# Kernel tuning notes

Measured on AMD Instinct MI355X. Metric: run time of the kernel, lower is better.

The kernel has to match this reference:

```python
import jax, jax.numpy as jnp
import numpy as np

WS = (5, 3, 1)          # per-level window sizes (CrossLayerPosEmbedding3D default)
STRIDES = (4, 2, 1)
PADS = (2, 1, 0)
HWS = (80, 40, 20)      # per-level map sizes -> 20x20 = 400 windows per level
B, C, NH = 8, 256, 4
HD = C // NH            # head_dim = 64
NTOK = (25, 9, 1)       # tokens per level, total 35
W0 = WS[0]
TABLE = (2 * W0 - 1) ** 2  # 81


def _rel_pos_index():
    # replicates CrossLayerPosEmbedding3D (spatial=True): float cross-scale coords
    coords = []
    for i, w in enumerate(WS):
        c = (np.arange(w) - w // 2).astype(np.float64)
        if i < len(WS) - 1:
            c = c * (W0 / w)
        gh, gw = np.meshgrid(c, c, indexing='ij')
        coords.append(np.stack([gh.reshape(-1), gw.reshape(-1)]))
    cf = np.concatenate(coords, axis=-1)                       # (2, 35)
    rel = (cf[:, :, None] - cf[:, None, :]).transpose(1, 2, 0).copy()
    rel[..., 0] += W0 - 1
    rel[..., 1] += W0 - 1
    rel[..., 0] *= 2 * W0 - 1
    return rel.sum(-1).astype(np.float32)                      # (35, 35) float index

REL_IDX = _rel_pos_index()
LEVEL_OF_TOKEN = np.repeat(np.arange(3), NTOK)                 # (35,)


def unfold(x, k, s, p):
    # torch.nn.functional.unfold -> (B, n_windows, k*k, C) (overlaped_window_partition)
    Bx, Cx, H, W = x.shape
    xp = jnp.pad(x, ((0, 0), (0, 0), (p, p), (p, p)))
    oh = (H + 2 * p - k) // s + 1
    ow = (W + 2 * p - k) // s + 1
    hi = (np.arange(oh) * s)[:, None] + np.arange(k)           # (oh, k)
    wi = (np.arange(ow) * s)[:, None] + np.arange(k)           # (ow, k)
    pt = xp[:, :, hi[:, None, :, None], wi[None, :, None, :]]  # (B, C, oh, ow, k, k)
    return pt.transpose(0, 2, 3, 4, 5, 1).reshape(Bx, oh * ow, k * k, Cx)


def fold(win, H, W, k, s, p):
    # torch.nn.functional.fold (sums overlaps) (overlaped_window_reverse)
    Bx, Wm, _, Cx = win.shape
    oh = (H + 2 * p - k) // s + 1
    ow = (W + 2 * p - k) // s + 1
    Hp, Wp = H + 2 * p, W + 2 * p
    hi = (np.arange(oh) * s)[:, None] + np.arange(k)
    wi = (np.arange(ow) * s)[:, None] + np.arange(k)
    lin = (hi[:, None, :, None] * Wp + wi[None, :, None, :]).reshape(-1)
    vals = win.transpose(0, 3, 1, 2).reshape(Bx, Cx, -1)       # matches (Wm, k*k) flatten order
    canvas = jnp.zeros((Bx, Cx, Hp * Wp), win.dtype).at[:, :, lin].add(vals)
    return canvas.reshape(Bx, Cx, Hp, Wp)[:, :, p:p + H, p:p + W]


def _l2n(x):
    # F.normalize(dim=-1), eps=1e-12
    return x / jnp.maximum(jnp.linalg.norm(x, axis=-1, keepdims=True), 1e-12)


def _forward(x0, x1, x2, w_qkv0, w_qkv1, w_qkv2, w_proj, b_proj, rpb_table, abs_bias):
    xs = (x0, x1, x2)
    wq = (w_qkv0, w_qkv1, w_qkv2)
    qs, ks, vs = [], [], []
    for l in range(3):  # small fixed layer loop (structurally distinct weights)
        t = unfold(xs[l], WS[l], STRIDES[l], PADS[l])          # (B, 400, ws^2, C)
        qkv = jnp.einsum('bwtc,cf->bwtf', t, wq[l])
        Bx, Wm, T, _ = qkv.shape
        qkv = qkv.reshape(Bx, Wm, T, 3, NH, HD).transpose(3, 0, 4, 1, 2, 5)  # (3,B,H,Wm,t,hd)
        qs.append(qkv[0]); ks.append(qkv[1]); vs.append(qkv[2])
    q = jnp.concatenate(qs, axis=-2)                           # (B, H, 400, 35, hd)
    k = jnp.concatenate(ks, axis=-2)
    v = jnp.concatenate(vs, axis=-2)

    # interpolated cross-layer relative position bias (floor/ceil lerp on the table)
    idx = jnp.asarray(REL_IDX.reshape(-1))
    fl = jnp.clip(jnp.floor(idx).astype(jnp.int32), 0, TABLE - 1)
    ce = jnp.clip(jnp.ceil(idx).astype(jnp.int32), 0, TABLE - 1)
    wce = (idx - fl.astype(jnp.float32))[:, None]
    pos = (1.0 - wce) * rpb_table[fl] + wce * rpb_table[ce]    # (1225, NH)
    pos = pos.reshape(sum(NTOK), sum(NTOK), NH).transpose(2, 0, 1)  # (NH, 35, 35)
    # per-level absolute bias added on query-row blocks (torch cat over dim=-2)
    pos = pos + abs_bias[LEVEL_OF_TOKEN].T[:, :, None]

    attn = jnp.einsum('bhwqd,bhwkd->bhwqk', _l2n(q), _l2n(k)) + pos[None, :, None]
    attn = jax.nn.softmax(attn, axis=-1)
    out = jnp.einsum('bhwqk,bhwkd->bhwqd', attn, v)            # (B, H, 400, 35, hd)
    Bx = out.shape[0]
    out = out.transpose(0, 2, 3, 1, 4).reshape(Bx, -1, sum(NTOK), NH * HD)  # (B,400,35,C)
    out = jnp.einsum('bwtc,cf->bwtf', out, w_proj) + b_proj
    outs = jnp.split(out, np.cumsum(NTOK)[:-1].tolist(), axis=2)
    return tuple(fold(o, HWS[l], HWS[l], WS[l], STRIDES[l], PADS[l])
                 for l, o in enumerate(outs))


def setup_inputs() -> dict:
    key = jax.random.key(0)
    ks = jax.random.split(key, 8)
    return {
        'x0': jax.random.normal(ks[0], (B, C, 80, 80), jnp.float32),
        'x1': jax.random.normal(ks[1], (B, C, 40, 40), jnp.float32),
        'x2': jax.random.normal(ks[2], (B, C, 20, 20), jnp.float32),
        'w_qkv0': jax.random.normal(ks[3], (C, 3 * C), jnp.float32) * 0.02,
        'w_qkv1': jax.random.normal(ks[4], (C, 3 * C), jnp.float32) * 0.02,
        'w_qkv2': jax.random.normal(ks[5], (C, 3 * C), jnp.float32) * 0.02,
        'w_proj': jax.random.normal(ks[6], (C, C), jnp.float32) * 0.02,
        'b_proj': jnp.zeros((C,), jnp.float32),
        'rpb_table': jax.random.normal(ks[7], (TABLE, NH), jnp.float32) * 0.02,
        'abs_bias': jnp.zeros((3, NH), jnp.float32),
    }


def reference(x0, x1, x2, w_qkv0, w_qkv1, w_qkv2, w_proj, b_proj, rpb_table, abs_bias):
    return _forward(x0, x1, x2, w_qkv0, w_qkv1, w_qkv2, w_proj, b_proj, rpb_table, abs_bias)
```

## Files before the change

kernel.cpp:

```cpp
#include <hip/hip_runtime.h>
#include <math.h>

namespace {

typedef _Float16 half8v __attribute__((ext_vector_type(8)));
typedef _Float16 half4v __attribute__((ext_vector_type(4)));
typedef float    floatx4 __attribute__((ext_vector_type(4)));

constexpr int B   = 8;
constexpr int C   = 256;
constexpr int NH  = 4;
constexpr int HD  = 64;
constexpr int NWIN = 400;
constexpr int NT  = 35;
constexpr int QKVN = 768;
constexpr int RPB = NWIN * NT;

constexpr size_t QKV_B  = (size_t)8400 * QKVN * 2;
constexpr size_t OATT_B = (size_t)RPB * C * 2;
constexpr size_t YT_B   = (size_t)RPB * C * 4;
constexpr size_t PB_B   = QKV_B + OATT_B + YT_B;
constexpr size_t POS_B  = 19712;

__device__ inline unsigned pack2(float a, float b) {
  union { _Float16 h[2]; unsigned u; } x;
  x.h[0] = (_Float16)a; x.h[1] = (_Float16)b;
  return x.u;
}

__device__ inline void token_coord(int j, double& cy, double& cx) {
  if (j < 25)      { int ty = j / 5,  tx = j % 5;  cy = (double)(ty - 2); cx = (double)(tx - 2); }
  else if (j < 34) { int t = j - 25; int ty = t / 3, tx = t % 3;
                     cy = (double)(ty - 1) * (5.0 / 3.0); cx = (double)(tx - 1) * (5.0 / 3.0); }
  else             { cy = 0.0; cx = 0.0; }
}

__global__ void pos_kernel(const float* __restrict__ rpb, const float* __restrict__ ab,
                           float* __restrict__ pos) {
  int p = blockIdx.x * blockDim.x + threadIdx.x;
  if (p >= NH * NT * NT) return;
  int j = p % NT, i = (p / NT) % NT, h = p / (NT * NT);
  double cyi, cxi, cyj, cxj;
  token_coord(i, cyi, cxi);
  token_coord(j, cyj, cxj);
  float fidx = (float)(((cyi - cyj) + 4.0) * 9.0 + ((cxi - cxj) + 4.0));
  int fl = min(max((int)floorf(fidx), 0), 80);
  int ce = min(max((int)ceilf(fidx), 0), 80);
  float w = fidx - (float)fl;
  float pv = (1.0f - w) * rpb[fl * NH + h] + w * rpb[ce * NH + h];
  int li = (i < 25) ? 0 : ((i < 34) ? 1 : 2);
  pos[p] = pv + ab[li * NH + h];
}

__global__ __launch_bounds__(256) void qkv_gemm(const float* __restrict__ X,
                                                const float* __restrict__ W,
                                                _Float16* __restrict__ Y,
                                                int HW, int Mg, int normN) {
  __shared__ _Float16 As[128][40];
  __shared__ _Float16 Bs[128][40];
  const int tid  = threadIdx.x;
  const int m0   = blockIdx.x * 128;
  const int n0   = blockIdx.y * 128;
  const int w    = tid >> 6;
  const int lane = tid & 63;
  const int quad = lane >> 4;
  const int mn   = lane & 15;

  floatx4 acc[2][8] = {};
  for (int k0 = 0; k0 < C; k0 += 32) {
    float av[2][8], bv[2][8];
    int rl[2];
#pragma unroll
    for (int u = 0; u < 2; ++u) {
      int c = w * 2 + u;
      int ko = c & 3;
      rl[u] = (c >> 2) * 64 + lane;
      int gm = min(m0 + rl[u], Mg - 1);
      int bb = gm / HW, pix = gm - bb * HW;
      const float* xp = X + ((size_t)bb * C + k0 + ko * 8) * HW + pix;
#pragma unroll
      for (int j = 0; j < 8; ++j) av[u][j] = xp[(size_t)j * HW];
      const float* wp = W + (size_t)(k0 + ko * 8) * QKVN + n0 + rl[u];
#pragma unroll
      for (int j = 0; j < 8; ++j) bv[u][j] = wp[(size_t)j * QKVN];
    }
#pragma unroll
    for (int u = 0; u < 2; ++u) {
      int ko = (w * 2 + u) & 3;
      half8v ha, hb;
#pragma unroll
      for (int j = 0; j < 8; ++j) { ha[j] = (_Float16)av[u][j]; hb[j] = (_Float16)bv[u][j]; }
      *(half8v*)&As[rl[u]][ko * 8] = ha;
      *(half8v*)&Bs[rl[u]][ko * 8] = hb;
    }
    __syncthreads();
    half8v a0 = *(const half8v*)&As[w * 32 + mn][quad * 8];
    half8v a1 = *(const half8v*)&As[w * 32 + 16 + mn][quad * 8];
#pragma unroll
    for (int ni = 0; ni < 8; ++ni) {
      half8v bf = *(const half8v*)&Bs[ni * 16 + mn][quad * 8];
      acc[0][ni] = __builtin_amdgcn_mfma_f32_16x16x32_f16(a0, bf, acc[0][ni], 0, 0, 0);
      acc[1][ni] = __builtin_amdgcn_mfma_f32_16x16x32_f16(a1, bf, acc[1][ni], 0, 0, 0);
    }
    __syncthreads();
  }

  const bool do_norm = (n0 < normN);
#pragma unroll
  for (int mi = 0; mi < 2; ++mi) {
#pragma unroll
    for (int r = 0; r < 4; ++r) {
      float s0 = 0.f, s1 = 0.f;
#pragma unroll
      for (int ni = 0; ni < 4; ++ni) { float vv = acc[mi][ni][r]; s0 += vv * vv; }
#pragma unroll
      for (int ni = 4; ni < 8; ++ni) { float vv = acc[mi][ni][r]; s1 += vv * vv; }
      s0 += __shfl_xor(s0, 1); s1 += __shfl_xor(s1, 1);
      s0 += __shfl_xor(s0, 2); s1 += __shfl_xor(s1, 2);
      s0 += __shfl_xor(s0, 4); s1 += __shfl_xor(s1, 4);
      s0 += __shfl_xor(s0, 8); s1 += __shfl_xor(s1, 8);
      float sc0 = do_norm ? (1.f / fmaxf(sqrtf(s0), 1e-12f)) : 1.f;
      float sc1 = do_norm ? (1.f / fmaxf(sqrtf(s1), 1e-12f)) : 1.f;
      int row = m0 + w * 32 + mi * 16 + quad * 4 + r;
      if (row < Mg) {
#pragma unroll
        for (int ni = 0; ni < 8; ++ni)
          Y[(size_t)row * QKVN + n0 + ni * 16 + mn] =
              (_Float16)(acc[mi][ni][r] * (ni < 4 ? sc0 : sc1));
      }
    }
  }
}

__device__ inline const _Float16* token_row_ptr(int j, int wy, int wx, int b,
                                                const _Float16* q0, const _Float16* q1,
                                                const _Float16* q2) {
  if (j >= NT) return nullptr;
  int k_, s_, p_, Hl, t; const _Float16* base;
  if (j < 25)      { k_ = 5; s_ = 4; p_ = 2; Hl = 80; t = j;      base = q0; }
  else if (j < 34) { k_ = 3; s_ = 2; p_ = 1; Hl = 40; t = j - 25; base = q1; }
  else             { k_ = 1; s_ = 1; p_ = 0; Hl = 20; t = 0;      base = q2; }
  int ty = t / k_, tx = t % k_;
  int y = wy * s_ + ty - p_;
  int x = wx * s_ + tx - p_;
  if ((unsigned)y >= (unsigned)Hl || (unsigned)x >= (unsigned)Hl) return nullptr;
  return base + ((size_t)b * Hl * Hl + (size_t)y * Hl + x) * QKVN;
}

__global__ __launch_bounds__(256, 4) void attn_kernel(const _Float16* __restrict__ qkv0,
                                                      const _Float16* __restrict__ qkv1,
                                                      const _Float16* __restrict__ qkv2,
                                                      const float* __restrict__ pos,
                                                      _Float16* __restrict__ O) {
  const int blk = blockIdx.x;
  const int w   = blk % NWIN;
  const int b   = blk / NWIN;
  const int wy = w / 20, wx = w % 20;
  const int tid  = threadIdx.x;
  const int h    = tid >> 6;
  const int lane = tid & 63;
  const int i16  = lane & 15;
  const int q4   = lane >> 4;

  __shared__ __align__(16) _Float16 vrows[48][260];

#pragma unroll
  for (int e0 = 0; e0 < 1536; e0 += 256) {
    int e = e0 + tid;
    int j = e >> 5, cc = e & 31;
    half8v val = (half8v)(_Float16)0.f;
    if (j < NT) {
      const _Float16* rp = token_row_ptr(j, wy, wx, b, qkv0, qkv1, qkv2);
      if (rp) val = *(const half8v*)(rp + 512 + cc * 8);
    }
    *(half8v*)&vrows[j][cc * 8] = val;
  }

  half8v qf[3][2], kf[3][2];
#pragma unroll
  for (int t = 0; t < 3; ++t) {
    const _Float16* rp = token_row_ptr(t * 16 + i16, wy, wx, b, qkv0, qkv1, qkv2);
#pragma unroll
    for (int kc = 0; kc < 2; ++kc) {
      if (rp) {
        qf[t][kc] = *(const half8v*)(rp + h * HD + kc * 32 + q4 * 8);
        kf[t][kc] = *(const half8v*)(rp + 256 + h * HD + kc * 32 + q4 * 8);
      } else {
        qf[t][kc] = (half8v)(_Float16)0.f;
        kf[t][kc] = (half8v)(_Float16)0.f;
      }
    }
  }

  floatx4 s[3][3] = {};
#pragma unroll
  for (int kc = 0; kc < 2; ++kc)
#pragma unroll
    for (int tj = 0; tj < 3; ++tj)
#pragma unroll
      for (int ti = 0; ti < 3; ++ti)
        s[tj][ti] = __builtin_amdgcn_mfma_f32_16x16x32_f16(kf[tj][kc], qf[ti][kc], s[tj][ti], 0, 0, 0);

#pragma unroll
  for (int tj = 0; tj < 3; ++tj)
#pragma unroll
    for (int ti = 0; ti < 3; ++ti)
#pragma unroll
      for (int r = 0; r < 4; ++r) {
        int j = tj * 16 + q4 * 4 + r;
        int i = ti * 16 + i16;
        if (j < NT) { if (i < NT) s[tj][ti][r] += pos[(h * NT + i) * NT + j]; }
        else s[tj][ti][r] = -INFINITY;
      }

  half4v pa[3][3];
#pragma unroll
  for (int ti = 0; ti < 3; ++ti) {
    float m = s[0][ti][0];
#pragma unroll
    for (int tj = 0; tj < 3; ++tj)
#pragma unroll
      for (int r = 0; r < 4; ++r) m = fmaxf(m, s[tj][ti][r]);
    m = fmaxf(m, __shfl_xor(m, 16));
    m = fmaxf(m, __shfl_xor(m, 32));
    float sum = 0.f;
#pragma unroll
    for (int tj = 0; tj < 3; ++tj)
#pragma unroll
      for (int r = 0; r < 4; ++r) { float e = expf(s[tj][ti][r] - m); s[tj][ti][r] = e; sum += e; }
    sum += __shfl_xor(sum, 16);
    sum += __shfl_xor(sum, 32);
    float inv = 1.f / sum;
#pragma unroll
    for (int tj = 0; tj < 3; ++tj)
#pragma unroll
      for (int r = 0; r < 4; ++r) pa[tj][ti][r] = (_Float16)(s[tj][ti][r] * inv);
  }

  __syncthreads();

  half4v vb[3][4];
#pragma unroll
  for (int tj = 0; tj < 3; ++tj)
#pragma unroll
    for (int n = 0; n < 4; ++n)
#pragma unroll
      for (int kk = 0; kk < 4; ++kk)
        vb[tj][n][kk] = vrows[tj * 16 + q4 * 4 + kk][h * HD + n * 16 + i16];

  const size_t obase = ((size_t)(b * NWIN + w) * NT) * C + h * HD;
#pragma unroll
  for (int ti = 0; ti < 3; ++ti) {
    floatx4 o[4] = {};
#pragma unroll
    for (int tj = 0; tj < 3; ++tj)
#pragma unroll
      for (int n = 0; n < 4; ++n)
        o[n] = __builtin_amdgcn_mfma_f32_16x16x16f16(pa[tj][ti], vb[tj][n], o[n], 0, 0, 0);
#pragma unroll
    for (int r = 0; r < 4; ++r) {
      int i = ti * 16 + q4 * 4 + r;
      if (i < NT) {
#pragma unroll
        for (int n = 0; n < 4; ++n)
          O[obase + (size_t)i * C + n * 16 + i16] = (_Float16)o[n][r];
      }
    }
  }
}

__global__ __launch_bounds__(256) void proj_gemm(const _Float16* __restrict__ A,
                                                 const float* __restrict__ W,
                                                 const float* __restrict__ bias,
                                                 float* __restrict__ Yt, int Mg) {
  __shared__ __align__(16) char smem[128 * 69 * 4];
  _Float16 (*As)[40] = (_Float16(*)[40])smem;
  _Float16 (*Bs)[40] = (_Float16(*)[40])(smem + 128 * 40 * 2);
  float    (*Cs)[69] = (float(*)[69])smem;

  const int tid  = threadIdx.x;
  const int m0   = blockIdx.x * 128;
  const int n0   = blockIdx.y * 64;
  const int w    = tid >> 6;
  const int lane = tid & 63;
  const int quad = lane >> 4;
  const int mn   = lane & 15;

  floatx4 acc[2][4] = {};
  for (int k0 = 0; k0 < C; k0 += 32) {
#pragma unroll
    for (int u = 0; u < 2; ++u) {
      int e = u * 256 + tid;
      int m = e >> 2, k8 = e & 3;
      int row = min(m0 + m, Mg - 1);
      half8v va = *(const half8v*)&A[(size_t)row * C + k0 + 8 * k8];
      *(half8v*)&As[m][8 * k8] = va;
    }
    {
      const float* wp = W + (size_t)(k0 + w * 8) * C + n0 + lane;
      float wv[8];
#pragma unroll
      for (int j = 0; j < 8; ++j) wv[j] = wp[(size_t)j * C];
      half8v hv;
#pragma unroll
      for (int j = 0; j < 8; ++j) hv[j] = (_Float16)wv[j];
      *(half8v*)&Bs[lane][w * 8] = hv;
    }
    __syncthreads();
    half8v a0 = *(const half8v*)&As[w * 32 + mn][quad * 8];
    half8v a1 = *(const half8v*)&As[w * 32 + 16 + mn][quad * 8];
#pragma unroll
    for (int ni = 0; ni < 4; ++ni) {
      half8v bf = *(const half8v*)&Bs[ni * 16 + mn][quad * 8];
      acc[0][ni] = __builtin_amdgcn_mfma_f32_16x16x32_f16(a0, bf, acc[0][ni], 0, 0, 0);
      acc[1][ni] = __builtin_amdgcn_mfma_f32_16x16x32_f16(a1, bf, acc[1][ni], 0, 0, 0);
    }
    __syncthreads();
  }

#pragma unroll
  for (int mi = 0; mi < 2; ++mi)
#pragma unroll
    for (int r = 0; r < 4; ++r)
#pragma unroll
      for (int ni = 0; ni < 4; ++ni)
        Cs[w * 32 + mi * 16 + quad * 4 + r][ni * 16 + mn] =
            acc[mi][ni][r] + bias[n0 + ni * 16 + mn];
  __syncthreads();
#pragma unroll
  for (int u = 0; u < 32; ++u) {
    int e = u * 256 + tid;
    int ml = e & 127, cl = e >> 7;
    int m = m0 + ml;
    if (m < Mg) {
      int bb = m / RPB;
      int r = m - bb * RPB;
      Yt[((size_t)bb * C + n0 + cl) * RPB + r] = Cs[ml][cl];
    }
  }
}

__global__ __launch_bounds__(256) void fold_kernel(const float* __restrict__ Yt,
                                                   float* __restrict__ out,
                                                   int k_, int s_, int p_, int H_,
                                                   int toff, int total) {
  int idx = blockIdx.x * 256 + threadIdx.x;
  if (idx >= total) return;
  int x = idx % H_;
  int y = (idx / H_) % H_;
  int c = (idx / (H_ * H_)) % C;
  int b = idx / (C * H_ * H_);
  int py = y + p_, px = x + p_;
  int ay = py - k_ + 1;
  int wy_lo = ay <= 0 ? 0 : (ay + s_ - 1) / s_;
  int wy_hi = min(19, py / s_);
  int ax = px - k_ + 1;
  int wx_lo = ax <= 0 ? 0 : (ax + s_ - 1) / s_;
  int wx_hi = min(19, px / s_);
  const float* base = Yt + ((size_t)b * C + c) * RPB;
  float acc = 0.f;
  for (int wy = wy_lo; wy <= wy_hi; ++wy) {
    int tyy = py - wy * s_;
    for (int wx = wx_lo; wx <= wx_hi; ++wx) {
      int txx = px - wx * s_;
      acc += base[(wy * 20 + wx) * NT + toff + tyy * k_ + txx];
    }
  }
  out[idx] = acc;
}

}

extern "C" void kernel_launch(void* const* d_in, const int* in_sizes, int n_in,
                              void* d_out, int out_size, void* d_ws, size_t ws_size,
                              hipStream_t stream) {
  const float* x0    = (const float*)d_in[0];
  const float* x1    = (const float*)d_in[1];
  const float* x2    = (const float*)d_in[2];
  const float* wq0   = (const float*)d_in[3];
  const float* wq1   = (const float*)d_in[4];
  const float* wq2   = (const float*)d_in[5];
  const float* wproj = (const float*)d_in[6];
  const float* bproj = (const float*)d_in[7];
  const float* rpb   = (const float*)d_in[8];
  const float* ab    = (const float*)d_in[9];
  float* out = (float*)d_out;

  int g = 8;
  while (g > 1 && POS_B + (size_t)g * PB_B > ws_size) g >>= 1;

  char* ws = (char*)d_ws;
  float*    posb  = (float*)ws;
  _Float16* qkv0g = (_Float16*)(ws + POS_B);
  _Float16* qkv1g = qkv0g + (size_t)g * 6400 * QKVN;
  _Float16* qkv2g = qkv1g + (size_t)g * 1600 * QKVN;
  _Float16* oatt  = qkv2g + (size_t)g *  400 * QKVN;
  float*    yt    = (float*)(ws + POS_B + (size_t)g * (QKV_B + OATT_B));

  pos_kernel<<<(NH * NT * NT + 255) / 256, 256, 0, stream>>>(rpb, ab, posb);

  const size_t off1 = (size_t)B * C * 6400;
  const size_t off2 = off1 + (size_t)B * C * 1600;

  for (int b0 = 0; b0 < B; b0 += g) {
    const float* x0g = x0 + (size_t)b0 * C * 6400;
    const float* x1g = x1 + (size_t)b0 * C * 1600;
    const float* x2g = x2 + (size_t)b0 * C * 400;

    qkv_gemm<<<dim3((g * 6400 + 127) / 128, QKVN / 128), 256, 0, stream>>>(x0g, wq0, qkv0g, 6400, g * 6400, 512);
    qkv_gemm<<<dim3((g * 1600 + 127) / 128, QKVN / 128), 256, 0, stream>>>(x1g, wq1, qkv1g, 1600, g * 1600, 512);
    qkv_gemm<<<dim3((g *  400 + 127) / 128, QKVN / 128), 256, 0, stream>>>(x2g, wq2, qkv2g,  400, g *  400, 512);

    attn_kernel<<<g * NWIN, 256, 0, stream>>>(qkv0g, qkv1g, qkv2g, posb, oatt);

    proj_gemm<<<dim3((g * RPB + 127) / 128, C / 64), 256, 0, stream>>>(oatt, wproj, bproj, yt, g * RPB);

    const int tot0 = g * C * 6400;
    const int tot1 = g * C * 1600;
    const int tot2 = g * C * 400;
    fold_kernel<<<(tot0 + 255) / 256, 256, 0, stream>>>(yt, out + (size_t)b0 * C * 6400,        5, 4, 2, 80, 0,  tot0);
    fold_kernel<<<(tot1 + 255) / 256, 256, 0, stream>>>(yt, out + off1 + (size_t)b0 * C * 1600, 3, 2, 1, 40, 25, tot1);
    fold_kernel<<<(tot2 + 255) / 256, 256, 0, stream>>>(yt, out + off2 + (size_t)b0 * C * 400,  1, 1, 0, 20, 34, tot2);
  }
}
```

Before: 493.5 us.

## Merge per-level QKV GEMMs into one launch and prefetch next K-tile in GEMMs

Combines the three per-level QKV GEMM launches into a single grid that picks its level's input, weights and output from the block index. This cuts launch overhead and lets the small level-1/2 tiles fill gaps alongside level 0. Both the QKV and projection GEMMs now load the next K-slice from global memory into registers while MFMAs run on the current LDS tile, so global latency is hidden behind compute. The cost is higher register pressure, which may reduce occupancy.

```diff
diff --git a/kernel.cpp b/kernel.cpp
--- a/kernel.cpp
+++ b/kernel.cpp
@@ -21,12 +21,6 @@
 constexpr size_t YT_B   = (size_t)RPB * C * 4;
 constexpr size_t PB_B   = QKV_B + OATT_B + YT_B;
 constexpr size_t POS_B  = 19712;
-
-__device__ inline unsigned pack2(float a, float b) {
-  union { _Float16 h[2]; unsigned u; } x;
-  x.h[0] = (_Float16)a; x.h[1] = (_Float16)b;
-  return x.u;
-}
 
 __device__ inline void token_coord(int j, double& cy, double& cx) {
   if (j < 25)      { int ty = j / 5,  tx = j % 5;  cy = (double)(ty - 2); cx = (double)(tx - 2); }
@@ -52,48 +46,72 @@
   pos[p] = pv + ab[li * NH + h];
 }
 
-__global__ __launch_bounds__(256) void qkv_gemm(const float* __restrict__ X,
-                                                const float* __restrict__ W,
-                                                _Float16* __restrict__ Y,
-                                                int HW, int Mg, int normN) {
+__global__ __launch_bounds__(256) void qkv_gemm(const float* __restrict__ X0,
+                                                const float* __restrict__ X1,
+                                                const float* __restrict__ X2,
+                                                const float* __restrict__ W0,
+                                                const float* __restrict__ W1,
+                                                const float* __restrict__ W2,
+                                                _Float16* __restrict__ Y0,
+                                                _Float16* __restrict__ Y1,
+                                                _Float16* __restrict__ Y2,
+                                                int mb0, int mb01, int g) {
   __shared__ _Float16 As[128][40];
   __shared__ _Float16 Bs[128][40];
+
+  int mblk = blockIdx.x;
+  const float* X; const float* W; _Float16* Y; int HW;
+  if (mblk < mb0)       { X = X0; W = W0; Y = Y0; HW = 6400; }
+  else if (mblk < mb01) { X = X1; W = W1; Y = Y1; HW = 1600; mblk -= mb0; }
+  else                  { X = X2; W = W2; Y = Y2; HW =  400; mblk -= mb01; }
+  const int Mg = g * HW;
+
   const int tid  = threadIdx.x;
-  const int m0   = blockIdx.x * 128;
+  const int m0   = mblk * 128;
   const int n0   = blockIdx.y * 128;
   const int w    = tid >> 6;
   const int lane = tid & 63;
   const int quad = lane >> 4;
   const int mn   = lane & 15;
 
+  int rl[2], koA[2];
+  const float* abase[2];
+  const float* bbase[2];
+#pragma unroll
+  for (int u = 0; u < 2; ++u) {
+    int c = w * 2 + u;
+    int ko = c & 3; koA[u] = ko;
+    rl[u] = (c >> 2) * 64 + lane;
+    int gm = min(m0 + rl[u], Mg - 1);
+    int bb = gm / HW, pix = gm - bb * HW;
+    abase[u] = X + ((size_t)bb * C + ko * 8) * HW + pix;
+    bbase[u] = W + (size_t)(ko * 8) * QKVN + n0 + rl[u];
+  }
+
+  float av[2][8], bv[2][8];
+  auto LOAD = [&](int k0) {
+#pragma unroll
+    for (int u = 0; u < 2; ++u) {
+      const float* xp = abase[u] + (size_t)k0 * HW;
+      const float* wp = bbase[u] + (size_t)k0 * QKVN;
+#pragma unroll
+      for (int j = 0; j < 8; ++j) { av[u][j] = xp[(size_t)j * HW]; bv[u][j] = wp[(size_t)j * QKVN]; }
+    }
+  };
+
+  LOAD(0);
   floatx4 acc[2][8] = {};
   for (int k0 = 0; k0 < C; k0 += 32) {
-    float av[2][8], bv[2][8];
-    int rl[2];
 #pragma unroll
     for (int u = 0; u < 2; ++u) {
-      int c = w * 2 + u;
-      int ko = c & 3;
-      rl[u] = (c >> 2) * 64 + lane;
-      int gm = min(m0 + rl[u], Mg - 1);
-      int bb = gm / HW, pix = gm - bb * HW;
-      const float* xp = X + ((size_t)bb * C + k0 + ko * 8) * HW + pix;
-#pragma unroll
-      for (int j = 0; j < 8; ++j) av[u][j] = xp[(size_t)j * HW];
-      const float* wp = W + (size_t)(k0 + ko * 8) * QKVN + n0 + rl[u];
-#pragma unroll
-      for (int j = 0; j < 8; ++j) bv[u][j] = wp[(size_t)j * QKVN];
-    }
-#pragma unroll
-    for (int u = 0; u < 2; ++u) {
-      int ko = (w * 2 + u) & 3;
       half8v ha, hb;
 #pragma unroll
       for (int j = 0; j < 8; ++j) { ha[j] = (_Float16)av[u][j]; hb[j] = (_Float16)bv[u][j]; }
-      *(half8v*)&As[rl[u]][ko * 8] = ha;
-      *(half8v*)&Bs[rl[u]][ko * 8] = hb;
+      *(half8v*)&As[rl[u]][koA[u] * 8] = ha;
+      *(half8v*)&Bs[rl[u]][koA[u] * 8] = hb;
     }
     __syncthreads();
+    if (k0 + 32 < C) LOAD(k0 + 32);
     half8v a0 = *(const half8v*)&As[w * 32 + mn][quad * 8];
     half8v a1 = *(const half8v*)&As[w * 32 + 16 + mn][quad * 8];
 #pragma unroll
@@ -105,7 +123,7 @@
     __syncthreads();
   }
 
-  const bool do_norm = (n0 < normN);
+  const bool do_norm = (n0 < 512);
 #pragma unroll
   for (int mi = 0; mi < 2; ++mi) {
 #pragma unroll
@@ -286,27 +304,37 @@
   const int quad = lane >> 4;
   const int mn   = lane & 15;
 
+  int aM[2], aK8[2], aRow[2];
+#pragma unroll
+  for (int u = 0; u < 2; ++u) {
+    int e = u * 256 + tid;
+    aM[u] = e >> 2; aK8[u] = e & 3;
+    aRow[u] = min(m0 + aM[u], Mg - 1);
+  }
+
+  half8v apre[2]; float bpre[8];
+  auto PLOAD = [&](int k0) {
+#pragma unroll
+    for (int u = 0; u < 2; ++u)
+      apre[u] = *(const half8v*)&A[(size_t)aRow[u] * C + k0 + 8 * aK8[u]];
+    const float* wp = W + (size_t)(k0 + w * 8) * C + n0 + lane;
+#pragma unroll
+    for (int j = 0; j < 8; ++j) bpre[j] = wp[(size_t)j * C];
+  };
+
+  PLOAD(0);
   floatx4 acc[2][4] = {};
   for (int k0 = 0; k0 < C; k0 += 32) {
 #pragma unroll
-    for (int u = 0; u < 2; ++u) {
-      int e = u * 256 + tid;
-      int m = e >> 2, k8 = e & 3;
-      int row = min(m0 + m, Mg - 1);
-      half8v va = *(const half8v*)&A[(size_t)row * C + k0 + 8 * k8];
-      *(half8v*)&As[m][8 * k8] = va;
-    }
+    for (int u = 0; u < 2; ++u) *(half8v*)&As[aM[u]][8 * aK8[u]] = apre[u];
     {
-      const float* wp = W + (size_t)(k0 + w * 8) * C + n0 + lane;
-      float wv[8];
-#pragma unroll
-      for (int j = 0; j < 8; ++j) wv[j] = wp[(size_t)j * C];
       half8v hv;
 #pragma unroll
-      for (int j = 0; j < 8; ++j) hv[j] = (_Float16)wv[j];
+      for (int j = 0; j < 8; ++j) hv[j] = (_Float16)bpre[j];
       *(half8v*)&Bs[lane][w * 8] = hv;
     }
     __syncthreads();
+    if (k0 + 32 < C) PLOAD(k0 + 32);
     half8v a0 = *(const half8v*)&As[w * 32 + mn][quad * 8];
     half8v a1 = *(const half8v*)&As[w * 32 + 16 + mn][quad * 8];
 #pragma unroll
@@ -402,14 +430,17 @@
   const size_t off1 = (size_t)B * C * 6400;
   const size_t off2 = off1 + (size_t)B * C * 1600;
 
+  const int mb0 = (g * 6400 + 127) / 128;
+  const int mb1 = (g * 1600 + 127) / 128;
+  const int mb2 = (g *  400 + 127) / 128;
+
   for (int b0 = 0; b0 < B; b0 += g) {
     const float* x0g = x0 + (size_t)b0 * C * 6400;
     const float* x1g = x1 + (size_t)b0 * C * 1600;
     const float* x2g = x2 + (size_t)b0 * C * 400;
 
-    qkv_gemm<<<dim3((g * 6400 + 127) / 128, QKVN / 128), 256, 0, stream>>>(x0g, wq0, qkv0g, 6400, g * 6400, 512);
-    qkv_gemm<<<dim3((g * 1600 + 127) / 128, QKVN / 128), 256, 0, stream>>>(x1g, wq1, qkv1g, 1600, g * 1600, 512);
-    qkv_gemm<<<dim3((g *  400 + 127) / 128, QKVN / 128), 256, 0, stream>>>(x2g, wq2, qkv2g,  400, g *  400, 512);
+    qkv_gemm<<<dim3(mb0 + mb1 + mb2, QKVN / 128), 256, 0, stream>>>(
+        x0g, x1g, x2g, wq0, wq1, wq2, qkv0g, qkv1g, qkv2g, mb0, mb0 + mb1, g);
 
     attn_kernel<<<g * NWIN, 256, 0, stream>>>(qkv0g, qkv1g, qkv2g, posb, oatt);
 
```

After: 456.6 us. 1.08x faster.
